# Performance work log

Measured on AMD Instinct MI355X. Metric: run time of the kernel, lower is better.

## Reference

```python
import jax, jax.numpy as jnp
import numpy as np

DIM = 128
HID = 128


def setup_inputs() -> dict:
    key = jax.random.key(0)
    ks = jax.random.split(key, 7)
    x = jax.random.normal(ks[0], (1, 256, 512, DIM), dtype=jnp.float32)
    s = 1.0 / np.sqrt(DIM)
    return {
        "x": x,
        "ln_g": jnp.ones((DIM,), jnp.float32),
        "ln_b": jnp.zeros((DIM,), jnp.float32),
        "w_left": jax.random.normal(ks[1], (DIM, HID), jnp.float32) * s,
        "b_left": jnp.zeros((HID,), jnp.float32),
        "w_right": jax.random.normal(ks[2], (DIM, HID), jnp.float32) * s,
        "b_right": jnp.zeros((HID,), jnp.float32),
        "w_out": jax.random.normal(ks[3], (HID, DIM), jnp.float32) * (1.0 / np.sqrt(HID)),
        "b_out": jnp.zeros((DIM,), jnp.float32),
    }


def reference(x, ln_g, ln_b, w_left, b_left, w_right, b_right, w_out, b_out):
    # LayerNorm over last dim (eps matches torch default 1e-5)
    mu = jnp.mean(x, axis=-1, keepdims=True)
    var = jnp.mean(jnp.square(x - mu), axis=-1, keepdims=True)
    xn = (x - mu) * jax.lax.rsqrt(var + 1e-5) * ln_g + ln_b
    # dual projections: (b, m, i, h)
    left = jnp.einsum('bmid,dh->bmih', xn, w_left) + b_left
    right = jnp.einsum('bmjd,dh->bmjh', xn, w_right) + b_right
    # mean over m of (left_i + right_j) == mean_m(left)_i + mean_m(right)_j
    # (exact algebraic identity; avoids the (b,m,i,j,h) intermediate)
    left_m = jnp.mean(left, axis=1)   # (b, i, h)
    right_m = jnp.mean(right, axis=1)  # (b, j, h)
    outer = left_m[:, :, None, :] + right_m[:, None, :, :]  # (b, i, j, h)
    return jnp.einsum('bijh,hd->bijd', outer, w_out) + b_out
```

## Files before the change

### kernel.cpp

```cpp
#include <hip/hip_runtime.h>
#include <hip/hip_bf16.h>


#define DIM 128
#define NI  512
#define NM  256

typedef float vfloat4 __attribute__((ext_vector_type(4)));

__global__ __launch_bounds__(512) void ln_proj_kernel(
    const float* __restrict__ x,
    const float* __restrict__ ln_g,
    const float* __restrict__ ln_b,
    const float* __restrict__ w_left,  const float* __restrict__ b_left,
    const float* __restrict__ w_right, const float* __restrict__ b_right,
    const float* __restrict__ w_out,   const float* __restrict__ b_out,
    float* __restrict__ L, float* __restrict__ R)
{
    const int i      = blockIdx.x;
    const int tid    = threadIdx.x;
    const int lane32 = tid & 31;
    const int grp    = tid >> 5;

    const vfloat4 g4 = *(const vfloat4*)(ln_g + 4 * lane32);
    const vfloat4 e4 = *(const vfloat4*)(ln_b + 4 * lane32);

    float a0 = 0.f, a1 = 0.f, a2 = 0.f, a3 = 0.f;
    const vfloat4* __restrict__ x4 = (const vfloat4*)x;

    #pragma unroll 4
    for (int t = 0; t < NM / 16; ++t) {
        const int m = grp + (t << 4);
        const vfloat4 v = x4[((size_t)(m * NI + i) << 5) + lane32];

        float s  = v.x + v.y + v.z + v.w;
        float s2 = v.x*v.x + v.y*v.y + v.z*v.z + v.w*v.w;
        #pragma unroll
        for (int off = 16; off; off >>= 1) {
            s  += __shfl_xor(s,  off);
            s2 += __shfl_xor(s2, off);
        }
        const float mu   = s * (1.f/128.f);
        const float rstd = rsqrtf(s2 * (1.f/128.f) - mu*mu + 1e-5f);

        a0 += (v.x - mu) * rstd * g4.x + e4.x;
        a1 += (v.y - mu) * rstd * g4.y + e4.y;
        a2 += (v.z - mu) * rstd * g4.z + e4.z;
        a3 += (v.w - mu) * rstd * g4.w + e4.w;
    }

    __shared__ vfloat4 sacc[512];
    __shared__ float   sS[DIM];
    __shared__ float   sT[2 * DIM];

    vfloat4 mine;
    mine.x = a0; mine.y = a1; mine.z = a2; mine.w = a3;
    sacc[tid] = mine;
    __syncthreads();

    if (tid < 32) {
        vfloat4 t = sacc[tid];
        #pragma unroll
        for (int gg = 1; gg < 16; ++gg)
            t += sacc[(gg << 5) + tid];
        const float inv = 1.f / (float)NM;
        sS[4*tid + 0] = t.x * inv;
        sS[4*tid + 1] = t.y * inv;
        sS[4*tid + 2] = t.z * inv;
        sS[4*tid + 3] = t.w * inv;
    }
    __syncthreads();

    if (tid < 256) {
        const int  h   = tid & 127;
        const bool isR = (tid >= 128);
        const float* __restrict__ W = isR ? w_right : w_left;
        float acc = isR ? b_right[h] : b_left[h];
        #pragma unroll 8
        for (int d = 0; d < DIM; ++d)
            acc += sS[d] * W[(d << 7) + h];
        sT[tid] = acc;
    }
    __syncthreads();

    if (tid < 256) {
        const int  h   = tid & 127;
        const bool isR = (tid >= 128);
        const float* __restrict__ T = isR ? (sT + DIM) : sT;
        float acc = isR ? b_out[h] : 0.f;
        #pragma unroll 8
        for (int hh = 0; hh < DIM; ++hh)
            acc += T[hh] * w_out[(hh << 7) + h];
        (isR ? R : L)[((size_t)i << 7) + h] = acc;
    }
}

__global__ __launch_bounds__(512) void expand_kernel(
    const vfloat4* __restrict__ L4,
    const vfloat4* __restrict__ R4,
    vfloat4* __restrict__ out4)
{
    const int i  = blockIdx.x;
    const int d4 = threadIdx.x & 31;
    const int jg = threadIdx.x >> 5;

    const vfloat4 l = L4[(i << 5) + d4];
    vfloat4* __restrict__ outb = out4 + ((size_t)i << 14);

    #pragma unroll 4
    for (int it = 0; it < 32; ++it) {
        const int j = jg + (it << 4);
        const vfloat4 r = R4[(j << 5) + d4];
        const vfloat4 o = l + r;
        __builtin_nontemporal_store(o, &outb[(j << 5) + d4]);
    }
}

extern "C" void kernel_launch(void* const* d_in, const int* in_sizes, int n_in,
                              void* d_out, int out_size, void* d_ws, size_t ws_size,
                              hipStream_t stream) {
    const float* x       = (const float*)d_in[0];
    const float* ln_g    = (const float*)d_in[1];
    const float* ln_b    = (const float*)d_in[2];
    const float* w_left  = (const float*)d_in[3];
    const float* b_left  = (const float*)d_in[4];
    const float* w_right = (const float*)d_in[5];
    const float* b_right = (const float*)d_in[6];
    const float* w_out   = (const float*)d_in[7];
    const float* b_out   = (const float*)d_in[8];

    float* L = (float*)d_ws;
    float* R = L + NI * DIM;

    ln_proj_kernel<<<NI, 512, 0, stream>>>(x, ln_g, ln_b,
                                           w_left, b_left, w_right, b_right,
                                           w_out, b_out, L, R);
    expand_kernel<<<NI, 512, 0, stream>>>((const vfloat4*)L,
                                          (const vfloat4*)R,
                                          (vfloat4*)d_out);
}
```

Measured before the change: 213.0 us.

## Fuse projection and expand kernels via cooperative grid sync

Merges the LayerNorm/projection kernel and the broadcast-add expand kernel into a single cooperative kernel that uses a grid-wide barrier. The left vector now stays in shared memory and only the right vector goes through global memory. This removes one kernel launch and a global round trip for L. In exchange it depends on all 512 blocks being co-resident, pays the cost of a grid-sync barrier, and goes through the cooperative launch path.

```diff
diff --git a/kernel.cpp b/kernel.cpp
--- a/kernel.cpp
+++ b/kernel.cpp
@@ -1,5 +1,8 @@
 #include <hip/hip_runtime.h>
 #include <hip/hip_bf16.h>
+#include <hip/hip_cooperative_groups.h>
+
+namespace cg = cooperative_groups;
 
 
 #define DIM 128
@@ -8,14 +11,15 @@
 
 typedef float vfloat4 __attribute__((ext_vector_type(4)));
 
-__global__ __launch_bounds__(512) void ln_proj_kernel(
+__global__ __launch_bounds__(512) void outer_mean_fused(
     const float* __restrict__ x,
     const float* __restrict__ ln_g,
     const float* __restrict__ ln_b,
     const float* __restrict__ w_left,  const float* __restrict__ b_left,
     const float* __restrict__ w_right, const float* __restrict__ b_right,
     const float* __restrict__ w_out,   const float* __restrict__ b_out,
-    float* __restrict__ L, float* __restrict__ R)
+    float* __restrict__ Rbuf,
+    vfloat4* __restrict__ out4)
 {
     const int i      = blockIdx.x;
     const int tid    = threadIdx.x;
@@ -52,6 +56,7 @@
     __shared__ vfloat4 sacc[512];
     __shared__ float   sS[DIM];
     __shared__ float   sT[2 * DIM];
+    __shared__ float   sL[DIM];
 
     vfloat4 mine;
     mine.x = a0; mine.y = a1; mine.z = a2; mine.w = a3;
@@ -72,10 +77,10 @@
     __syncthreads();
 
     if (tid < 256) {
-        const int  h   = tid & 127;
-        const bool isR = (tid >= 128);
-        const float* __restrict__ W = isR ? w_right : w_left;
-        float acc = isR ? b_right[h] : b_left[h];
+        const int  h     = tid & 127;
+        const bool right = (tid < 128);
+        const float* __restrict__ W = right ? w_right : w_left;
+        float acc = right ? b_right[h] : b_left[h];
         #pragma unroll 8
         for (int d = 0; d < DIM; ++d)
             acc += sS[d] * W[(d << 7) + h];
@@ -84,35 +89,30 @@
     __syncthreads();
 
     if (tid < 256) {
-        const int  h   = tid & 127;
-        const bool isR = (tid >= 128);
-        const float* __restrict__ T = isR ? (sT + DIM) : sT;
-        float acc = isR ? b_out[h] : 0.f;
+        const int  h     = tid & 127;
+        const bool right = (tid < 128);
+        const float* __restrict__ T = right ? sT : (sT + DIM);
+        float acc = right ? b_out[h] : 0.f;
         #pragma unroll 8
         for (int hh = 0; hh < DIM; ++hh)
             acc += T[hh] * w_out[(hh << 7) + h];
-        (isR ? R : L)[((size_t)i << 7) + h] = acc;
+        if (right) Rbuf[((size_t)i << 7) + h] = acc;
+        else       sL[h] = acc;
     }
-}
 
-__global__ __launch_bounds__(512) void expand_kernel(
-    const vfloat4* __restrict__ L4,
-    const vfloat4* __restrict__ R4,
-    vfloat4* __restrict__ out4)
-{
-    const int i  = blockIdx.x;
-    const int d4 = threadIdx.x & 31;
-    const int jg = threadIdx.x >> 5;
+    __threadfence();
+    cg::this_grid().sync();
 
-    const vfloat4 l = L4[(i << 5) + d4];
+    const vfloat4* __restrict__ R4 = (const vfloat4*)Rbuf;
+    const vfloat4 l = *(const vfloat4*)(sL + 4 * lane32);
     vfloat4* __restrict__ outb = out4 + ((size_t)i << 14);
 
     #pragma unroll 4
     for (int it = 0; it < 32; ++it) {
-        const int j = jg + (it << 4);
-        const vfloat4 r = R4[(j << 5) + d4];
+        const int j = grp + (it << 4);
+        const vfloat4 r = R4[(j << 5) + lane32];
         const vfloat4 o = l + r;
-        __builtin_nontemporal_store(o, &outb[(j << 5) + d4]);
+        __builtin_nontemporal_store(o, &outb[(j << 5) + lane32]);
     }
 }
 
@@ -129,13 +129,16 @@
     const float* w_out   = (const float*)d_in[7];
     const float* b_out   = (const float*)d_in[8];
 
-    float* L = (float*)d_ws;
-    float* R = L + NI * DIM;
+    float*   R    = (float*)d_ws;
+    vfloat4* out4 = (vfloat4*)d_out;
 
-    ln_proj_kernel<<<NI, 512, 0, stream>>>(x, ln_g, ln_b,
-                                           w_left, b_left, w_right, b_right,
-                                           w_out, b_out, L, R);
-    expand_kernel<<<NI, 512, 0, stream>>>((const vfloat4*)L,
-                                          (const vfloat4*)R,
-                                          (vfloat4*)d_out);
+    void* args[] = {
+        (void*)&x, (void*)&ln_g, (void*)&ln_b,
+        (void*)&w_left, (void*)&b_left,
+        (void*)&w_right, (void*)&b_right,
+        (void*)&w_out, (void*)&b_out,
+        (void*)&R, (void*)&out4,
+    };
+    hipLaunchCooperativeKernel((const void*)outer_mean_fused,
+                               dim3(NI), dim3(512), args, 0, stream);
 }
```

Result: slower. 332.6 us (+56.1%).
